# Kernel optimization log

Hardware: AMD Instinct MI355X
Metric: run time of the kernel (lower is better)

## Reference

```python
import jax, jax.numpy as jnp
import numpy as np

B, C, N, Fd = 8, 64, 256, 128
EPS = 1e-5


def setup_inputs() -> dict:
    key = jax.random.key(0)
    k_h, k_op, k_s, k_q = jax.random.split(key, 4)
    # xavier_uniform bound for [C, 2F, 1] slices: gain*sqrt(6/(fan_in+fan_out)) with fan_in=2F, fan_out=1
    bound = float(np.sqrt(6.0 / (2 * Fd + 1)))
    h = jax.random.normal(k_h, (B, C, N, Fd), dtype=jnp.float32)
    op = jax.random.uniform(k_op, (C, 2 * Fd, 1), minval=-bound, maxval=bound, dtype=jnp.float32)
    op_S = jax.random.uniform(k_s, (C, 2 * Fd, 1), minval=-bound, maxval=bound, dtype=jnp.float32)
    op_Q = jax.random.uniform(k_q, (C, 2 * Fd, 1), minval=-bound, maxval=bound, dtype=jnp.float32)
    gamma = jnp.ones((C,), dtype=jnp.float32)
    beta = jnp.zeros((C,), dtype=jnp.float32)
    return {"h": h, "op": op, "op_S": op_S, "op_Q": op_Q, "gamma": gamma, "beta": beta}


def reference(h, op, op_S, op_Q, gamma, beta):
    # h: [B, C, N, F]
    source = h[:, :, 0:1, :]                              # [B,C,1,F]
    h_src = jnp.broadcast_to(source, h.shape)             # repeat_interleave over N
    h_op = jnp.concatenate([h_src, h], axis=-1)           # [B,C,N,2F]
    # [B,C,N,2F] x [C,2F,1] -> [B,C,N,1]
    attn_op = jax.nn.sigmoid(jnp.einsum('bcnf,cfo->bcno', h_op, op))
    op_mask = (attn_op >= 0.5).astype(h.dtype)            # hard threshold (no grad)
    supp = h * op_mask                                    # [B,C,N,F]
    query = h * (1.0 - op_mask)
    supp_mean = jnp.mean(supp, axis=2, keepdims=True)     # [B,C,1,F]
    query_mean = jnp.mean(query, axis=2, keepdims=True)
    supp_attn = jnp.einsum('bcnf,cfo->bcno', jnp.concatenate([supp_mean, source], axis=-1), op_S)
    query_attn = jnp.einsum('bcnf,cfo->bcno', jnp.concatenate([query_mean, source], axis=-1), op_Q)
    op_attn = jax.nn.softmax(jnp.concatenate([supp_attn, query_attn], axis=-1), axis=-1)  # [B,C,1,2]
    h_opn = supp * op_attn[..., 0:1] + query * op_attn[..., 1:2]  # [B,C,N,F]
    # BatchNorm2d (training-mode batch stats) over (B,N,F) per channel
    mean = jnp.mean(h_opn, axis=(0, 2, 3), keepdims=True)
    var = jnp.var(h_opn, axis=(0, 2, 3), keepdims=True)
    h_bn = (h_opn - mean) * jax.lax.rsqrt(var + EPS)
    h_bn = h_bn * gamma[None, :, None, None] + beta[None, :, None, None]
    return jax.nn.elu(h_bn)
```

## Files before the change

kernel.cpp:

```cpp
#include <hip/hip_runtime.h>
#include <math.h>

#define Bb 8
#define Cc 64
#define Nn 256
#define FD 128
#define SEGS 4
#define ROWS 64
#define TILE (Nn * FD)

typedef float floatx4 __attribute__((ext_vector_type(4)));

__global__ __launch_bounds__(256) void s1(
    const float* __restrict__ h, const float* __restrict__ op,
    const float* __restrict__ opS, const float* __restrict__ opQ,
    unsigned long long* __restrict__ maskbuf, float* __restrict__ bpart) {
  const int blk = blockIdx.x;
  const int bc = blk >> 2, seg = blk & 3;
  const int c = bc & (Cc - 1);
  const float* __restrict__ tile = h + (size_t)bc * TILE;
  const int tid = threadIdx.x, lane = tid & 63, wv = tid >> 6;
  const int hw = tid >> 5, hl = tid & 31;

  __shared__ float s_dh[ROWS];
  __shared__ float s_red[4][6];
  __shared__ float s_cs;

  if (wv == 0) {
    const float* __restrict__ opc = op + c * 2 * FD;
    float a = tile[lane], b = tile[lane + 64];
    float cs = a * opc[lane] + b * opc[lane + 64];
#pragma unroll
    for (int off = 32; off >= 1; off >>= 1) cs += __shfl_xor(cs, off, 64);
    if (lane == 0) s_cs = cs;
  }

  const float4 oH = ((const float4*)(op  + c * 2 * FD + FD))[hl];
  const float4 oS = ((const float4*)(opS + c * 2 * FD))[hl];
  const float4 oQ = ((const float4*)(opQ + c * 2 * FD))[hl];

  float dsp[8], dqp[8], rsp[8], rssp[8];

#pragma unroll
  for (int i = 0; i < 8; ++i) {
    const int nl = hw * 8 + i;
    const float4 v = ((const float4*)(tile + (size_t)(seg * ROWS + nl) * FD))[hl];
    float dh = v.x * oH.x + v.y * oH.y + v.z * oH.z + v.w * oH.w;
    dsp[i]  = v.x * oS.x + v.y * oS.y + v.z * oS.z + v.w * oS.w;
    dqp[i]  = v.x * oQ.x + v.y * oQ.y + v.z * oQ.z + v.w * oQ.w;
    rsp[i]  = v.x + v.y + v.z + v.w;
    rssp[i] = v.x * v.x + v.y * v.y + v.z * v.z + v.w * v.w;
#pragma unroll
    for (int off = 16; off >= 1; off >>= 1) dh += __shfl_xor(dh, off, 64);
    if (hl == 0) s_dh[nl] = dh;
  }
  __syncthreads();

  const float cs = s_cs;

  if (wv == 0) {
    const bool m = (s_dh[lane] + cs) >= 0.0f;
    const unsigned long long bits = __ballot(m);
    if (lane == 0) maskbuf[blk] = bits;
  }

  float a_ds = 0, a_dq = 0, a_rsm = 0, a_rsq = 0, a_rssm = 0, a_rssq = 0;
#pragma unroll
  for (int i = 0; i < 8; ++i) {
    const bool m = (s_dh[hw * 8 + i] + cs) >= 0.0f;
    a_ds   += m ? dsp[i]  : 0.0f;
    a_dq   += m ? 0.0f    : dqp[i];
    a_rsm  += m ? rsp[i]  : 0.0f;
    a_rsq  += m ? 0.0f    : rsp[i];
    a_rssm += m ? rssp[i] : 0.0f;
    a_rssq += m ? 0.0f    : rssp[i];
  }
#pragma unroll
  for (int off = 32; off >= 1; off >>= 1) {
    a_ds   += __shfl_xor(a_ds,   off, 64);
    a_dq   += __shfl_xor(a_dq,   off, 64);
    a_rsm  += __shfl_xor(a_rsm,  off, 64);
    a_rsq  += __shfl_xor(a_rsq,  off, 64);
    a_rssm += __shfl_xor(a_rssm, off, 64);
    a_rssq += __shfl_xor(a_rssq, off, 64);
  }
  if (lane == 0) {
    s_red[wv][0] = a_ds;  s_red[wv][1] = a_dq;
    s_red[wv][2] = a_rsm; s_red[wv][3] = a_rsq;
    s_red[wv][4] = a_rssm; s_red[wv][5] = a_rssq;
  }
  __syncthreads();
  if (tid < 6) {
    bpart[(size_t)blk * 8 + tid] =
        s_red[0][tid] + s_red[1][tid] + s_red[2][tid] + s_red[3][tid];
  }
}

__global__ __launch_bounds__(256) void s2f(
    const float* __restrict__ h, const unsigned long long* __restrict__ maskbuf,
    const float* __restrict__ bpart, const float* __restrict__ opS,
    const float* __restrict__ opQ, const float* __restrict__ gamma,
    const float* __restrict__ beta, float* __restrict__ out) {
  const int blk = blockIdx.x, bc = blk >> 2, seg = blk & 3;
  const int c = bc & (Cc - 1), bmine = bc >> 6;
  const int tid = threadIdx.x, lane = tid & 63, hw = tid >> 5, hl = tid & 31;
  __shared__ float s_S[Bb], s_SS[Bb], s_ws[2 * Bb];
  __shared__ float s_a[ROWS];

  const int b = hw;
  const int bcb = b * Cc + c;

  const float4 s4 = ((const float4*)(h + (size_t)bcb * TILE))[hl];
  const float4 oS = ((const float4*)(opS + c * 2 * FD + FD))[hl];
  const float4 oQ = ((const float4*)(opQ + c * 2 * FD + FD))[hl];
  float ss = s4.x * oS.x + s4.y * oS.y + s4.z * oS.z + s4.w * oS.w;
  float qq = s4.x * oQ.x + s4.y * oQ.y + s4.z * oQ.z + s4.w * oQ.w;
#pragma unroll
  for (int off = 16; off >= 1; off >>= 1) {
    ss += __shfl_xor(ss, off, 64);
    qq += __shfl_xor(qq, off, 64);
  }

  float aj = 0.0f;
  if (hl < 6) {
#pragma unroll
    for (int k = 0; k < SEGS; ++k)
      aj += bpart[(size_t)(bcb * SEGS + k) * 8 + hl];
  }
  const int base = lane & 32;
  float a0 = __shfl(aj, base + 0, 64), a1 = __shfl(aj, base + 1, 64);
  float a2 = __shfl(aj, base + 2, 64), a3 = __shfl(aj, base + 3, 64);
  float a4 = __shfl(aj, base + 4, 64), a5 = __shfl(aj, base + 5, 64);

  float sa = a0 * (1.0f / Nn) + ss;
  float qa = a1 * (1.0f / Nn) + qq;
  float mx = fmaxf(sa, qa);
  float es = __expf(sa - mx), eq = __expf(qa - mx);
  float inv = 1.0f / (es + eq);
  float w_s = es * inv, w_q = eq * inv;
  if (hl == 0) {
    s_S[b]  = w_s * a2 + w_q * a3;
    s_SS[b] = w_s * w_s * a4 + w_q * w_q * a5;
    s_ws[2 * b] = w_s; s_ws[2 * b + 1] = w_q;
  }
  __syncthreads();

  float S = 0.0f, SS = 0.0f;
#pragma unroll
  for (int k = 0; k < Bb; ++k) { S += s_S[k]; SS += s_SS[k]; }
  const float invcnt = 1.0f / (float)(Bb * Nn * FD);
  const float mean = S * invcnt;
  const float var  = SS * invcnt - mean * mean;
  const float scale = gamma[c] * rsqrtf(var + 1e-5f);
  const float shift = beta[c] - mean * scale;

  if (tid < ROWS) {
    const unsigned long long m = maskbuf[blk];
    const float w = ((m >> tid) & 1ull) ? s_ws[2 * bmine] : s_ws[2 * bmine + 1];
    s_a[tid] = w * scale;
  }
  __syncthreads();

  const float4* __restrict__ h4 = (const float4*)(h + (size_t)bc * TILE) + seg * 2048;
  floatx4* __restrict__ o4 = (floatx4*)(out + (size_t)bc * TILE) + seg * 2048;
#pragma unroll
  for (int k = 0; k < 8; ++k) {
    const int idx = k * 256 + tid;
    const float a = s_a[idx >> 5];
    float4 v = h4[idx];
    floatx4 r;
    r.x = fmaf(v.x, a, shift);
    r.y = fmaf(v.y, a, shift);
    r.z = fmaf(v.z, a, shift);
    r.w = fmaf(v.w, a, shift);
    r.x = r.x > 0.0f ? r.x : __expf(r.x) - 1.0f;
    r.y = r.y > 0.0f ? r.y : __expf(r.y) - 1.0f;
    r.z = r.z > 0.0f ? r.z : __expf(r.z) - 1.0f;
    r.w = r.w > 0.0f ? r.w : __expf(r.w) - 1.0f;
    __builtin_nontemporal_store(r, &o4[idx]);
  }
}

extern "C" void kernel_launch(void* const* d_in, const int* in_sizes, int n_in,
                              void* d_out, int out_size, void* d_ws, size_t ws_size,
                              hipStream_t stream) {
  const float* h     = (const float*)d_in[0];
  const float* op    = (const float*)d_in[1];
  const float* opS   = (const float*)d_in[2];
  const float* opQ   = (const float*)d_in[3];
  const float* gamma = (const float*)d_in[4];
  const float* beta  = (const float*)d_in[5];
  float* out = (float*)d_out;

  unsigned long long* maskbuf = (unsigned long long*)d_ws;
  float* bpart = (float*)((char*)d_ws + 16384);

  s1<<<Bb * Cc * SEGS, 256, 0, stream>>>(h, op, opS, opQ, maskbuf, bpart);
  s2f<<<Bb * Cc * SEGS, 256, 0, stream>>>(h, maskbuf, bpart, opS, opQ, gamma, beta, out);
}
```

Measured before the change: 133.9 us.

## Fuse both passes into one persistent kernel with a grid-wide spin barrier

The two kernels become a single launch with one block per (b,c) tile. A global atomic counter acts as a grid barrier, replacing the inter-kernel boundary. The first quarter of each tile (32 KB) is cached in LDS for reuse in the output pass, and masks stay in shared memory instead of a global buffer. This cuts launch overhead and some rereads of h. In exchange, grid parallelism drops from 2048 to 512 blocks, and it relies on all 512 blocks being co-resident, or the spin barrier deadlocks.

```diff
diff --git a/kernel.cpp b/kernel.cpp
--- a/kernel.cpp
+++ b/kernel.cpp
@@ -5,31 +5,36 @@
 #define Cc 64
 #define Nn 256
 #define FD 128
-#define SEGS 4
 #define ROWS 64
 #define TILE (Nn * FD)
+#define GRID (Bb * Cc)
 
 typedef float floatx4 __attribute__((ext_vector_type(4)));
 
-__global__ __launch_bounds__(256) void s1(
+__global__ __launch_bounds__(256, 2) void fused(
     const float* __restrict__ h, const float* __restrict__ op,
     const float* __restrict__ opS, const float* __restrict__ opQ,
-    unsigned long long* __restrict__ maskbuf, float* __restrict__ bpart) {
-  const int blk = blockIdx.x;
-  const int bc = blk >> 2, seg = blk & 3;
-  const int c = bc & (Cc - 1);
+    const float* __restrict__ gamma, const float* __restrict__ beta,
+    float* __restrict__ bpart, unsigned int* __restrict__ counter,
+    float* __restrict__ out) {
+  const int bc = blockIdx.x;
+  const int c = bc & (Cc - 1), bmine = bc >> 6;
   const float* __restrict__ tile = h + (size_t)bc * TILE;
   const int tid = threadIdx.x, lane = tid & 63, wv = tid >> 6;
   const int hw = tid >> 5, hl = tid & 31;
 
+  __shared__ float4 s_cache[2048];
   __shared__ float s_dh[ROWS];
+  __shared__ unsigned long long s_mask[4];
   __shared__ float s_red[4][6];
   __shared__ float s_cs;
+  __shared__ float s_S[Bb], s_SS[Bb], s_ws[2 * Bb];
+  __shared__ float s_a[Nn];
 
   if (wv == 0) {
     const float* __restrict__ opc = op + c * 2 * FD;
-    float a = tile[lane], b = tile[lane + 64];
-    float cs = a * opc[lane] + b * opc[lane + 64];
+    float a = tile[lane], b2 = tile[lane + 64];
+    float cs = a * opc[lane] + b2 * opc[lane + 64];
 #pragma unroll
     for (int off = 32; off >= 1; off >>= 1) cs += __shfl_xor(cs, off, 64);
     if (lane == 0) s_cs = cs;
@@ -38,43 +43,51 @@
   const float4 oH = ((const float4*)(op  + c * 2 * FD + FD))[hl];
   const float4 oS = ((const float4*)(opS + c * 2 * FD))[hl];
   const float4 oQ = ((const float4*)(opQ + c * 2 * FD))[hl];
-
-  float dsp[8], dqp[8], rsp[8], rssp[8];
-
-#pragma unroll
-  for (int i = 0; i < 8; ++i) {
-    const int nl = hw * 8 + i;
-    const float4 v = ((const float4*)(tile + (size_t)(seg * ROWS + nl) * FD))[hl];
-    float dh = v.x * oH.x + v.y * oH.y + v.z * oH.z + v.w * oH.w;
-    dsp[i]  = v.x * oS.x + v.y * oS.y + v.z * oS.z + v.w * oS.w;
-    dqp[i]  = v.x * oQ.x + v.y * oQ.y + v.z * oQ.z + v.w * oQ.w;
-    rsp[i]  = v.x + v.y + v.z + v.w;
-    rssp[i] = v.x * v.x + v.y * v.y + v.z * v.z + v.w * v.w;
-#pragma unroll
-    for (int off = 16; off >= 1; off >>= 1) dh += __shfl_xor(dh, off, 64);
-    if (hl == 0) s_dh[nl] = dh;
-  }
-  __syncthreads();
-
-  const float cs = s_cs;
-
-  if (wv == 0) {
-    const bool m = (s_dh[lane] + cs) >= 0.0f;
-    const unsigned long long bits = __ballot(m);
-    if (lane == 0) maskbuf[blk] = bits;
-  }
+  const float4* __restrict__ tile4 = (const float4*)tile;
 
   float a_ds = 0, a_dq = 0, a_rsm = 0, a_rsq = 0, a_rssm = 0, a_rssq = 0;
-#pragma unroll
-  for (int i = 0; i < 8; ++i) {
-    const bool m = (s_dh[hw * 8 + i] + cs) >= 0.0f;
-    a_ds   += m ? dsp[i]  : 0.0f;
-    a_dq   += m ? 0.0f    : dqp[i];
-    a_rsm  += m ? rsp[i]  : 0.0f;
-    a_rsq  += m ? 0.0f    : rsp[i];
-    a_rssm += m ? rssp[i] : 0.0f;
-    a_rssq += m ? 0.0f    : rssp[i];
-  }
+
+  for (int seg = 0; seg < 4; ++seg) {
+    float4 v[8];
+#pragma unroll
+    for (int i = 0; i < 8; ++i)
+      v[i] = tile4[(size_t)(seg * ROWS + hw * 8 + i) * 32 + hl];
+    if (seg == 0) {
+#pragma unroll
+      for (int i = 0; i < 8; ++i) s_cache[(hw * 8 + i) * 32 + hl] = v[i];
+    }
+    float dsp[8], dqp[8], rsp[8], rssp[8];
+#pragma unroll
+    for (int i = 0; i < 8; ++i) {
+      float dh = v[i].x * oH.x + v[i].y * oH.y + v[i].z * oH.z + v[i].w * oH.w;
+      dsp[i]  = v[i].x * oS.x + v[i].y * oS.y + v[i].z * oS.z + v[i].w * oS.w;
+      dqp[i]  = v[i].x * oQ.x + v[i].y * oQ.y + v[i].z * oQ.z + v[i].w * oQ.w;
+      rsp[i]  = v[i].x + v[i].y + v[i].z + v[i].w;
+      rssp[i] = v[i].x * v[i].x + v[i].y * v[i].y + v[i].z * v[i].z + v[i].w * v[i].w;
+#pragma unroll
+      for (int off = 16; off >= 1; off >>= 1) dh += __shfl_xor(dh, off, 64);
+      if (hl == 0) s_dh[hw * 8 + i] = dh;
+    }
+    __syncthreads();
+    const float cs = s_cs;
+    if (wv == 0) {
+      const bool m = (s_dh[lane] + cs) >= 0.0f;
+      const unsigned long long bits = __ballot(m);
+      if (lane == 0) s_mask[seg] = bits;
+    }
+#pragma unroll
+    for (int i = 0; i < 8; ++i) {
+      const bool m = (s_dh[hw * 8 + i] + cs) >= 0.0f;
+      a_ds   += m ? dsp[i]  : 0.0f;
+      a_dq   += m ? 0.0f    : dqp[i];
+      a_rsm  += m ? rsp[i]  : 0.0f;
+      a_rsq  += m ? 0.0f    : rsp[i];
+      a_rssm += m ? rssp[i] : 0.0f;
+      a_rssq += m ? 0.0f    : rssp[i];
+    }
+    __syncthreads();
+  }
+
 #pragma unroll
   for (int off = 32; off >= 1; off >>= 1) {
     a_ds   += __shfl_xor(a_ds,   off, 64);
@@ -85,48 +98,42 @@
     a_rssq += __shfl_xor(a_rssq, off, 64);
   }
   if (lane == 0) {
-    s_red[wv][0] = a_ds;  s_red[wv][1] = a_dq;
-    s_red[wv][2] = a_rsm; s_red[wv][3] = a_rsq;
-    s_red[wv][4] = a_rssm; s_red[wv][5] = a_rssq;
+    s_red[wv][0] = a_ds;  s_red[wv][1] = a_dq;  s_red[wv][2] = a_rsm;
+    s_red[wv][3] = a_rsq; s_red[wv][4] = a_rssm; s_red[wv][5] = a_rssq;
   }
   __syncthreads();
   if (tid < 6) {
-    bpart[(size_t)blk * 8 + tid] =
+    bpart[(size_t)bc * 8 + tid] =
         s_red[0][tid] + s_red[1][tid] + s_red[2][tid] + s_red[3][tid];
   }
-}
-
-__global__ __launch_bounds__(256) void s2f(
-    const float* __restrict__ h, const unsigned long long* __restrict__ maskbuf,
-    const float* __restrict__ bpart, const float* __restrict__ opS,
-    const float* __restrict__ opQ, const float* __restrict__ gamma,
-    const float* __restrict__ beta, float* __restrict__ out) {
-  const int blk = blockIdx.x, bc = blk >> 2, seg = blk & 3;
-  const int c = bc & (Cc - 1), bmine = bc >> 6;
-  const int tid = threadIdx.x, lane = tid & 63, hw = tid >> 5, hl = tid & 31;
-  __shared__ float s_S[Bb], s_SS[Bb], s_ws[2 * Bb];
-  __shared__ float s_a[ROWS];
-
+
+  __threadfence();
+  __syncthreads();
+  if (tid == 0) {
+    atomicAdd(counter, 1u);
+    while (__hip_atomic_load(counter, __ATOMIC_ACQUIRE,
+                             __HIP_MEMORY_SCOPE_AGENT) < (unsigned)GRID) {
+      __builtin_amdgcn_s_sleep(8);
+    }
+    __threadfence();
+  }
+  __syncthreads();
+
+  volatile const float* bp = bpart;
   const int b = hw;
   const int bcb = b * Cc + c;
-
   const float4 s4 = ((const float4*)(h + (size_t)bcb * TILE))[hl];
-  const float4 oS = ((const float4*)(opS + c * 2 * FD + FD))[hl];
-  const float4 oQ = ((const float4*)(opQ + c * 2 * FD + FD))[hl];
-  float ss = s4.x * oS.x + s4.y * oS.y + s4.z * oS.z + s4.w * oS.w;
-  float qq = s4.x * oQ.x + s4.y * oQ.y + s4.z * oQ.z + s4.w * oQ.w;
+  const float4 oSs = ((const float4*)(opS + c * 2 * FD + FD))[hl];
+  const float4 oQs = ((const float4*)(opQ + c * 2 * FD + FD))[hl];
+  float ss = s4.x * oSs.x + s4.y * oSs.y + s4.z * oSs.z + s4.w * oSs.w;
+  float qq = s4.x * oQs.x + s4.y * oQs.y + s4.z * oQs.z + s4.w * oQs.w;
 #pragma unroll
   for (int off = 16; off >= 1; off >>= 1) {
     ss += __shfl_xor(ss, off, 64);
     qq += __shfl_xor(qq, off, 64);
   }
-
   float aj = 0.0f;
-  if (hl < 6) {
-#pragma unroll
-    for (int k = 0; k < SEGS; ++k)
-      aj += bpart[(size_t)(bcb * SEGS + k) * 8 + hl];
-  }
+  if (hl < 6) aj = bp[(size_t)bcb * 8 + hl];
   const int base = lane & 32;
   float a0 = __shfl(aj, base + 0, 64), a1 = __shfl(aj, base + 1, 64);
   float a2 = __shfl(aj, base + 2, 64), a3 = __shfl(aj, base + 3, 64);
@@ -154,20 +161,20 @@
   const float scale = gamma[c] * rsqrtf(var + 1e-5f);
   const float shift = beta[c] - mean * scale;
 
-  if (tid < ROWS) {
-    const unsigned long long m = maskbuf[blk];
-    const float w = ((m >> tid) & 1ull) ? s_ws[2 * bmine] : s_ws[2 * bmine + 1];
-    s_a[tid] = w * scale;
-  }
-  __syncthreads();
-
-  const float4* __restrict__ h4 = (const float4*)(h + (size_t)bc * TILE) + seg * 2048;
-  floatx4* __restrict__ o4 = (floatx4*)(out + (size_t)bc * TILE) + seg * 2048;
+  {
+    const int r = tid;
+    const unsigned long long m = s_mask[r >> 6];
+    const float w = ((m >> (r & 63)) & 1ull) ? s_ws[2 * bmine] : s_ws[2 * bmine + 1];
+    s_a[r] = w * scale;
+  }
+  __syncthreads();
+
+  floatx4* __restrict__ o4 = (floatx4*)(out + (size_t)bc * TILE);
 #pragma unroll
   for (int k = 0; k < 8; ++k) {
     const int idx = k * 256 + tid;
     const float a = s_a[idx >> 5];
-    float4 v = h4[idx];
+    float4 v = s_cache[idx];
     floatx4 r;
     r.x = fmaf(v.x, a, shift);
     r.y = fmaf(v.y, a, shift);
@@ -179,6 +186,22 @@
     r.w = r.w > 0.0f ? r.w : __expf(r.w) - 1.0f;
     __builtin_nontemporal_store(r, &o4[idx]);
   }
+#pragma unroll 4
+  for (int k = 8; k < 32; ++k) {
+    const int idx = k * 256 + tid;
+    const float a = s_a[idx >> 5];
+    float4 v = tile4[idx];
+    floatx4 r;
+    r.x = fmaf(v.x, a, shift);
+    r.y = fmaf(v.y, a, shift);
+    r.z = fmaf(v.z, a, shift);
+    r.w = fmaf(v.w, a, shift);
+    r.x = r.x > 0.0f ? r.x : __expf(r.x) - 1.0f;
+    r.y = r.y > 0.0f ? r.y : __expf(r.y) - 1.0f;
+    r.z = r.z > 0.0f ? r.z : __expf(r.z) - 1.0f;
+    r.w = r.w > 0.0f ? r.w : __expf(r.w) - 1.0f;
+    __builtin_nontemporal_store(r, &o4[idx]);
+  }
 }
 
 extern "C" void kernel_launch(void* const* d_in, const int* in_sizes, int n_in,
@@ -192,9 +215,10 @@
   const float* beta  = (const float*)d_in[5];
   float* out = (float*)d_out;
 
-  unsigned long long* maskbuf = (unsigned long long*)d_ws;
-  float* bpart = (float*)((char*)d_ws + 16384);
-
-  s1<<<Bb * Cc * SEGS, 256, 0, stream>>>(h, op, opS, opQ, maskbuf, bpart);
-  s2f<<<Bb * Cc * SEGS, 256, 0, stream>>>(h, maskbuf, bpart, opS, opQ, gamma, beta, out);
+  float* bpart = (float*)d_ws;
+  unsigned int* counter = (unsigned int*)((char*)d_ws + 16384);
+
+  hipMemsetAsync(counter, 0, sizeof(unsigned int), stream);
+  fused<<<GRID, 256, 0, stream>>>(h, op, opS, opQ, gamma, beta,
+                                  bpart, counter, out);
 }
```

After: 205.1 us. +53.2%, slower.
